# Performance work log

Measured on AMD Instinct MI355X. Metric: run time of the kernel, lower is better.

Reference implementation:

```python
import jax, jax.numpy as jnp
import numpy as np
import math

HIDDEN = 1024
HEADS = 16
HEAD_DIM = HIDDEN // HEADS


def setup_inputs() -> dict:
    key = jax.random.key(0)
    ks = jax.random.split(key, 7)
    B, S = 2, 2048
    scale = 1.0 / math.sqrt(HIDDEN)
    return {
        "x": jax.random.normal(ks[0], (B, S, HIDDEN), dtype=jnp.float32),
        "Wq": jax.random.normal(ks[1], (HIDDEN, HIDDEN), dtype=jnp.float32) * scale,
        "Wk": jax.random.normal(ks[2], (HIDDEN, HIDDEN), dtype=jnp.float32) * scale,
        "Wv": jax.random.normal(ks[3], (HIDDEN, HIDDEN), dtype=jnp.float32) * scale,
        "Wo": jax.random.normal(ks[4], (HIDDEN, HIDDEN), dtype=jnp.float32) * scale,
        "quantum_phase": jax.random.normal(ks[5], (HEADS, HEAD_DIM), dtype=jnp.float32),
        "quantum_amplitude": jnp.ones((HEADS, HEAD_DIM), dtype=jnp.float32),
    }


def reference(x, Wq, Wk, Wv, Wo, quantum_phase, quantum_amplitude):
    B, S, d = x.shape
    H, D = HEADS, HEAD_DIM

    # per-head/per-channel quantum modulation: real(x*exp(i*phase)) == x*cos(phase)
    mod = (jnp.cos(quantum_phase) * quantum_amplitude)[None, :, None, :]  # [1,H,1,D]

    def proj(W):
        return (x @ W).reshape(B, S, H, D).transpose(0, 2, 1, 3)  # [B,H,S,D]

    q = proj(Wq) * mod
    k = proj(Wk) * mod
    v = proj(Wv) * mod

    scores = jnp.einsum("bhid,bhjd->bhij", q, k) / math.sqrt(D)  # [B,H,S,S]

    # quantum interference: scores[i,j] *= cos(2*pi*(i-j)/S)
    idx = jnp.arange(S, dtype=jnp.float32)
    cos_mat = jnp.cos(2.0 * math.pi * (idx[:, None] - idx[None, :]) / S)  # [S,S]
    scores = scores * cos_mat

    w = jax.nn.softmax(scores, axis=-1)
    # superposition of attention weights with key-rolled copy
    w = (w + jnp.roll(w, 1, axis=-1)) / math.sqrt(2.0)

    out = jnp.einsum("bhij,bhjd->bhid", w, v)  # [B,H,S,D]
    out = out.transpose(0, 2, 1, 3).reshape(B, S, d)
    return out @ Wo
```

## Files before the change

kernel.cpp:

```cpp
#include <hip/hip_runtime.h>
#include <hip/hip_bf16.h>
#include <math.h>

#define HIDDEN 1024
#define HEADS  16
#define HDIM   64
#define BATCH  2
#define SEQ    2048
#define ROWS   (BATCH*SEQ)
#define BH     (BATCH*HEADS)

typedef __attribute__((ext_vector_type(8))) short  short8;
typedef __attribute__((ext_vector_type(8))) __bf16 bf16x8;
typedef __attribute__((ext_vector_type(4))) float  f32x4;

static __device__ __forceinline__ unsigned short f2bf(float f) {
    unsigned int u = __builtin_bit_cast(unsigned int, f);
    u += 0x7FFFu + ((u >> 16) & 1u);
    return (unsigned short)(u >> 16);
}
static __device__ __forceinline__ float bf2f(unsigned short h) {
    unsigned int u = ((unsigned int)h) << 16;
    return __builtin_bit_cast(float, u);
}
static __device__ __forceinline__ f32x4 mfma16(short8 a, short8 b, f32x4 c) {
    return __builtin_amdgcn_mfma_f32_16x16x32_bf16(
        __builtin_bit_cast(bf16x8, a), __builtin_bit_cast(bf16x8, b), c, 0, 0, 0);
}
static __device__ __forceinline__ void gl_lds16(const unsigned short* g, unsigned short* l) {
    __builtin_amdgcn_global_load_lds(
        (const __attribute__((address_space(1))) unsigned int*)g,
        (__attribute__((address_space(3))) unsigned int*)l, 16, 0, 0);
}

__global__ __launch_bounds__(256) void prep_kernel(
    const float* __restrict__ x, unsigned short* __restrict__ xb,
    const float* __restrict__ w0, const float* __restrict__ w1,
    const float* __restrict__ w2, const float* __restrict__ w3,
    unsigned short* __restrict__ wt,
    const float* __restrict__ qp, const float* __restrict__ qa,
    float* __restrict__ mod, float* __restrict__ mod2,
    float* __restrict__ posc, float* __restrict__ poss) {
    __shared__ unsigned short tile[64][72];
    const int bid = blockIdx.x;
    const int t = threadIdx.x;
    if (bid < 4096) {
        int i = (bid * 256 + t) * 4;
        float4 v = *(const float4*)(x + i);
        ushort4 o;
        o.x = f2bf(v.x); o.y = f2bf(v.y); o.z = f2bf(v.z); o.w = f2bf(v.w);
        *(ushort4*)(xb + i) = o;
        if (bid < 8) {
            int k = bid * 256 + t;
            if (k < HIDDEN) {
                float m = cosf(qp[k]) * qa[k];
                mod[k] = m;
                mod2[k] = m * m * 0.18033688011112042f;
            }
            if (k < SEQ) {
                float ang = (float)k * (6.283185307179586f / (float)SEQ);
                posc[k] = cosf(ang);
                poss[k] = sinf(ang);
            }
        }
        return;
    }
    int rem = bid - 4096;
    int z = rem >> 8, r2 = rem & 255;
    int n0 = (r2 & 15) * 64, k0 = (r2 >> 4) * 64;
    const float* src = (z == 0) ? w0 : (z == 1) ? w1 : (z == 2) ? w2 : w3;
    unsigned short* dst = wt + (size_t)z * HIDDEN * HIDDEN;
    int cg = t & 15, r0 = t >> 4;
#pragma unroll
    for (int rr = 0; rr < 4; rr++) {
        int kl = r0 + rr * 16;
        float4 v = *(const float4*)(src + (size_t)(k0 + kl) * HIDDEN + n0 + cg * 4);
        tile[cg*4+0][kl] = f2bf(v.x);
        tile[cg*4+1][kl] = f2bf(v.y);
        tile[cg*4+2][kl] = f2bf(v.z);
        tile[cg*4+3][kl] = f2bf(v.w);
    }
    __syncthreads();
#pragma unroll
    for (int rr = 0; rr < 4; rr++) {
        int nl = r0 + rr * 16;
        ushort4 o;
        o.x = tile[nl][cg*4+0]; o.y = tile[nl][cg*4+1];
        o.z = tile[nl][cg*4+2]; o.w = tile[nl][cg*4+3];
        *(ushort4*)(dst + (size_t)(n0 + nl) * HIDDEN + k0 + cg * 4) = o;
    }
}

__global__ __launch_bounds__(256) void gemm_kernel(
    const unsigned short* __restrict__ A, const unsigned short* __restrict__ WtBase,
    unsigned short* __restrict__ CBase, const float* __restrict__ mod) {
    __shared__ unsigned short Alds[128 * 64];
    __shared__ unsigned short Blds[128 * 64];
    const int mode = blockIdx.z;
    const unsigned short* Bt = WtBase + (size_t)mode * HIDDEN * HIDDEN;
    unsigned short* Cout = CBase + (size_t)mode * ROWS * HIDDEN;
    const int m0 = blockIdx.x * 128, n0 = blockIdx.y * 128;
    const int tid = threadIdx.x;
    const int wave = tid >> 6, lane = tid & 63, quad = lane >> 4, l15 = lane & 15;
    const int wr = wave >> 1, wc = wave & 1;
    const int srow = lane >> 3;
    const int schunk = (lane & 7) ^ (srow & 7);

    f32x4 acc[4][4];
    const f32x4 z4 = {0.f, 0.f, 0.f, 0.f};
#pragma unroll
    for (int i = 0; i < 4; i++)
#pragma unroll
        for (int j = 0; j < 4; j++) acc[i][j] = z4;

    for (int k0 = 0; k0 < HIDDEN; k0 += 64) {
#pragma unroll
        for (int p = 0; p < 4; p++) {
            int rbase = p * 32 + wave * 8;
            gl_lds16(A  + (size_t)(m0 + rbase + srow) * HIDDEN + k0 + schunk * 8,
                     &Alds[rbase * 64]);
            gl_lds16(Bt + (size_t)(n0 + rbase + srow) * HIDDEN + k0 + schunk * 8,
                     &Blds[rbase * 64]);
        }
        __syncthreads();
        short8 aF[4][2], bF[4][2];
#pragma unroll
        for (int h = 0; h < 2; h++) {
#pragma unroll
            for (int i = 0; i < 4; i++) {
                int row = wr * 64 + i * 16 + l15;
                aF[i][h] = *(const short8*)(&Alds[row * 64 + ((h * 4 + quad) ^ (l15 & 7)) * 8]);
            }
#pragma unroll
            for (int j = 0; j < 4; j++) {
                int row = wc * 64 + j * 16 + l15;
                bF[j][h] = *(const short8*)(&Blds[row * 64 + ((h * 4 + quad) ^ (l15 & 7)) * 8]);
            }
        }
#pragma unroll
        for (int h = 0; h < 2; h++)
#pragma unroll
            for (int i = 0; i < 4; i++)
#pragma unroll
                for (int j = 0; j < 4; j++)
                    acc[i][j] = mfma16(aF[i][h], bF[j][h], acc[i][j]);
        __syncthreads();
    }

#pragma unroll
    for (int i = 0; i < 4; i++) {
        int mbase = m0 + wr * 64 + i * 16 + quad * 4;
#pragma unroll
        for (int j = 0; j < 4; j++) {
            int n = n0 + wc * 64 + j * 16 + l15;
            float vm = (mode == 2) ? mod[n] : 1.0f;
#pragma unroll
            for (int r = 0; r < 4; r++) {
                int mm = mbase + r;
                Cout[(size_t)mm * HIDDEN + n] = f2bf(acc[i][j][r] * vm);
            }
        }
    }
}

__global__ __launch_bounds__(256) void gemm_o_kernel(
    const unsigned short* __restrict__ A, const unsigned short* __restrict__ Bt,
    float* __restrict__ Out) {
    __shared__ unsigned short Alds[128 * 64];
    __shared__ unsigned short Blds[64 * 64];
    const int m0 = blockIdx.x * 128, n0 = blockIdx.y * 64;
    const int tid = threadIdx.x;
    const int wave = tid >> 6, lane = tid & 63, quad = lane >> 4, l15 = lane & 15;
    const int wr = wave >> 1, wc = wave & 1;
    const int srow = lane >> 3;
    const int schunk = (lane & 7) ^ (srow & 7);

    f32x4 acc[4][2];
    const f32x4 z4 = {0.f, 0.f, 0.f, 0.f};
#pragma unroll
    for (int i = 0; i < 4; i++)
#pragma unroll
        for (int j = 0; j < 2; j++) acc[i][j] = z4;

    for (int k0 = 0; k0 < HIDDEN; k0 += 64) {
#pragma unroll
        for (int p = 0; p < 4; p++) {
            int rbase = p * 32 + wave * 8;
            gl_lds16(A + (size_t)(m0 + rbase + srow) * HIDDEN + k0 + schunk * 8,
                     &Alds[rbase * 64]);
        }
#pragma unroll
        for (int p = 0; p < 2; p++) {
            int rbase = p * 32 + wave * 8;
            gl_lds16(Bt + (size_t)(n0 + rbase + srow) * HIDDEN + k0 + schunk * 8,
                     &Blds[rbase * 64]);
        }
        __syncthreads();
        short8 aF[4][2], bF[2][2];
#pragma unroll
        for (int h = 0; h < 2; h++) {
#pragma unroll
            for (int i = 0; i < 4; i++) {
                int row = wr * 64 + i * 16 + l15;
                aF[i][h] = *(const short8*)(&Alds[row * 64 + ((h * 4 + quad) ^ (l15 & 7)) * 8]);
            }
#pragma unroll
            for (int j = 0; j < 2; j++) {
                int row = wc * 32 + j * 16 + l15;
                bF[j][h] = *(const short8*)(&Blds[row * 64 + ((h * 4 + quad) ^ (l15 & 7)) * 8]);
            }
        }
#pragma unroll
        for (int h = 0; h < 2; h++)
#pragma unroll
            for (int i = 0; i < 4; i++)
#pragma unroll
                for (int j = 0; j < 2; j++)
                    acc[i][j] = mfma16(aF[i][h], bF[j][h], acc[i][j]);
        __syncthreads();
    }

#pragma unroll
    for (int i = 0; i < 4; i++) {
        int mbase = m0 + wr * 64 + i * 16 + quad * 4;
#pragma unroll
        for (int j = 0; j < 2; j++) {
            int n = n0 + wc * 32 + j * 16 + l15;
#pragma unroll
            for (int r = 0; r < 4; r++)
                Out[(size_t)(mbase + r) * HIDDEN + n] = acc[i][j][r];
        }
    }
}

__global__ __launch_bounds__(256) void vshift_kernel(const unsigned short* __restrict__ Vm,
                                                     unsigned short* __restrict__ Vpt) {
    __shared__ unsigned short lds[65][72];
    int bh = blockIdx.x, b = bh >> 4, h = bh & 15;
    int s0 = blockIdx.y * 64;
    int t = threadIdx.x;
    int cg = t & 15, r0 = t >> 4;
#pragma unroll
    for (int rr = 0; rr < 4; rr++) {
        int row = r0 + rr * 16;
        ushort4 v = *(const ushort4*)(Vm + ((size_t)(b * SEQ + s0 + row)) * HIDDEN + h * 64 + cg * 4);
        *(ushort4*)(&lds[row][cg * 4]) = v;
    }
    if (t < 16) {
        int srow = (s0 + 64) & (SEQ - 1);
        ushort4 v = *(const ushort4*)(Vm + ((size_t)(b * SEQ + srow)) * HIDDEN + h * 64 + t * 4);
        *(ushort4*)(&lds[64][t * 4]) = v;
    }
    __syncthreads();
    int d = t & 63, sb = (t >> 6) * 16;
    unsigned short outv[16];
#pragma unroll
    for (int k = 0; k < 16; k++) {
        float a = bf2f(lds[sb + k][d]), bb = bf2f(lds[sb + k + 1][d]);
        outv[k] = f2bf((a + bb) * 0.7071067811865476f);
    }
    unsigned short* dst = Vpt + ((size_t)bh * 64 + d) * SEQ + s0 + sb;
#pragma unroll
    for (int k = 0; k < 16; k += 4) {
        ushort4 o; o.x = outv[k]; o.y = outv[k+1]; o.z = outv[k+2]; o.w = outv[k+3];
        *(ushort4*)(dst + k) = o;
    }
}

#define KT 64
#define PSTR 76
__global__ __launch_bounds__(256) void attn_kernel(const unsigned short* __restrict__ Cq,
                                                   const unsigned short* __restrict__ Ck,
                                                   const unsigned short* __restrict__ Vpt,
                                                   unsigned short* __restrict__ Ob,
                                                   const float* __restrict__ mod2,
                                                   const float* __restrict__ posc,
                                                   const float* __restrict__ poss) {
    __shared__ unsigned short Klds[2][KT * 64];
    __shared__ unsigned short Vtlds[2][64 * 64];
    __shared__ unsigned short Plds[4 * 32 * PSTR];
    const int bh = blockIdx.x;
    const int b = bh >> 4, h = bh & 15;
    const int tid = threadIdx.x, wave = tid >> 6, lane = tid & 63;
    const int quad = lane >> 4, l15 = lane & 15;
    const int q0 = blockIdx.y * 128 + wave * 32;

    short8 qf[2][2];
#pragma unroll
    for (int g = 0; g < 2; g++) {
        int ss = q0 + g * 16 + l15;
        const unsigned short* crow = Cq + ((size_t)(b * SEQ + ss)) * HIDDEN + h * 64;
#pragma unroll
        for (int kk = 0; kk < 2; kk++) {
            int bd = kk * 32 + quad * 8;
            short8 u = *(const short8*)(crow + bd);
            short8 q;
#pragma unroll
            for (int e = 0; e < 8; e++)
                q[e] = (short)f2bf(bf2f((unsigned short)u[e]) * mod2[h * 64 + bd + e]);
            qf[g][kk] = q;
        }
    }
    float ci[2][4], si[2][4];
#pragma unroll
    for (int g = 0; g < 2; g++)
#pragma unroll
        for (int r = 0; r < 4; r++) {
            int ss = q0 + g * 16 + quad * 4 + r;
            ci[g][r] = posc[ss];
            si[g][r] = poss[ss];
        }

    short8 ones;
#pragma unroll
    for (int e = 0; e < 8; e++) ones[e] = (short)0x3F80;

    const f32x4 z4 = {0.f, 0.f, 0.f, 0.f};
    f32x4 acc[2][4], accden[2];
#pragma unroll
    for (int g = 0; g < 2; g++) {
#pragma unroll
        for (int dt = 0; dt < 4; dt++) acc[g][dt] = z4;
        accden[g] = z4;
    }

    unsigned short* pw = &Plds[wave * 32 * PSTR];

    const unsigned short* Kbh = Ck  + ((size_t)b * SEQ) * HIDDEN + h * 64;
    const unsigned short* Vbh = Vpt + (size_t)bh * 64 * SEQ;

    auto stage = [&](int j, int buf) {
#pragma unroll
        for (int p = 0; p < 2; p++) {
            int rb = p * 32 + wave * 8;
            int r  = rb + (lane >> 3);
            int c  = (lane & 7) ^ (r & 7);
            gl_lds16(Kbh + (size_t)(j + r) * HIDDEN + c * 8, &Klds[buf][rb * 64]);
        }
#pragma unroll
        for (int p = 0; p < 2; p++) {
            int rb = p * 32 + wave * 8;
            int r  = rb + (lane >> 3);
            int c  = (lane & 7) ^ (r & 7);
            gl_lds16(Vbh + (size_t)r * SEQ + j + c * 8, &Vtlds[buf][rb * 64]);
        }
    };

    float cjc[4], sjc[4];
#pragma unroll
    for (int t2 = 0; t2 < 4; t2++) {
        int jj = t2 * 16 + l15;
        cjc[t2] = posc[jj]; sjc[t2] = poss[jj];
    }

    stage(0, 0);
    for (int it = 0; it < SEQ / KT; it++) {
        __syncthreads();
        float cjn[4] = {0.f, 0.f, 0.f, 0.f}, sjn[4] = {0.f, 0.f, 0.f, 0.f};
        if (it + 1 < SEQ / KT) {
            stage((it + 1) * KT, (it + 1) & 1);
#pragma unroll
            for (int t2 = 0; t2 < 4; t2++) {
                int jj = (it + 1) * KT + t2 * 16 + l15;
                cjn[t2] = posc[jj]; sjn[t2] = poss[jj];
            }
        }
        const int buf = it & 1;

#pragma unroll
        for (int t2 = 0; t2 < 4; t2++) {
            float cj = cjc[t2], sj = sjc[t2];
            f32x4 sc[2] = {z4, z4};
#pragma unroll
            for (int kk = 0; kk < 2; kk++) {
                int ch = (kk * 4 + quad) ^ (l15 & 7);
                short8 kf = *(const short8*)(&Klds[buf][(t2 * 16 + l15) * 64 + ch * 8]);
#pragma unroll
                for (int g = 0; g < 2; g++)
                    sc[g] = mfma16(qf[g][kk], kf, sc[g]);
            }
#pragma unroll
            for (int g = 0; g < 2; g++) {
#pragma unroll
                for (int r = 0; r < 4; r++) {
                    float w = ci[g][r] * cj + si[g][r] * sj;
                    float p = __builtin_amdgcn_exp2f(sc[g][r] * w);
                    unsigned short pt = (unsigned short)(__builtin_bit_cast(unsigned int, p) >> 16);
                    pw[(g * 16 + quad * 4 + r) * PSTR + t2 * 16 + l15] = pt;
                }
            }
        }

#pragma unroll
        for (int pt = 0; pt < 2; pt++) {
            short8 pa0 = *(const short8*)(&pw[(l15) * PSTR + pt * 32 + quad * 8]);
            short8 pa1 = *(const short8*)(&pw[(16 + l15) * PSTR + pt * 32 + quad * 8]);
            accden[0] = mfma16(pa0, ones, accden[0]);
            accden[1] = mfma16(pa1, ones, accden[1]);
#pragma unroll
            for (int dt = 0; dt < 4; dt++) {
                int ch = (pt * 4 + quad) ^ (l15 & 7);
                short8 vb = *(const short8*)(&Vtlds[buf][(dt * 16 + l15) * 64 + ch * 8]);
                acc[0][dt] = mfma16(pa0, vb, acc[0][dt]);
                acc[1][dt] = mfma16(pa1, vb, acc[1][dt]);
            }
        }
#pragma unroll
        for (int t2 = 0; t2 < 4; t2++) { cjc[t2] = cjn[t2]; sjc[t2] = sjn[t2]; }
    }

#pragma unroll
    for (int g = 0; g < 2; g++) {
        float rinv[4];
#pragma unroll
        for (int r = 0; r < 4; r++) rinv[r] = 1.0f / accden[g][r];
#pragma unroll
        for (int dt = 0; dt < 4; dt++) {
#pragma unroll
            for (int r = 0; r < 4; r++) {
                int q = q0 + g * 16 + quad * 4 + r;
                int d = dt * 16 + l15;
                Ob[((size_t)(b * SEQ + q)) * HIDDEN + h * 64 + d] = f2bf(acc[g][dt][r] * rinv[r]);
            }
        }
    }
}

extern "C" void kernel_launch(void* const* d_in, const int* in_sizes, int n_in,
                              void* d_out, int out_size, void* d_ws, size_t ws_size,
                              hipStream_t stream) {
    const float* x  = (const float*)d_in[0];
    const float* Wq = (const float*)d_in[1];
    const float* Wk = (const float*)d_in[2];
    const float* Wv = (const float*)d_in[3];
    const float* Wo = (const float*)d_in[4];
    const float* qp = (const float*)d_in[5];
    const float* qa = (const float*)d_in[6];
    char* ws = (char*)d_ws;

    unsigned short* Xb  = (unsigned short*)(ws);
    unsigned short* Wt  = (unsigned short*)(ws + (size_t)( 8 << 20));
    unsigned short* Cq  = (unsigned short*)(ws + (size_t)(16 << 20));
    unsigned short* Ck  = (unsigned short*)(ws + (size_t)(24 << 20));
    unsigned short* Cv  = (unsigned short*)(ws + (size_t)(32 << 20));
    unsigned short* Vpt = (unsigned short*)(ws + (size_t)(40 << 20));
    float* mod  = (float*)(ws + (size_t)(48 << 20));
    float* mod2 = mod + 1024;
    float* posc = mod2 + 1024;
    float* poss = posc + 2048;
    float* out  = (float*)d_out;

    prep_kernel<<<5120, 256, 0, stream>>>(x, Xb, Wq, Wk, Wv, Wo, Wt,
                                          qp, qa, mod, mod2, posc, poss);
    gemm_kernel<<<dim3(32, 8, 3), 256, 0, stream>>>(Xb, Wt, Cq, mod);
    vshift_kernel<<<dim3(32, 32), 256, 0, stream>>>(Cv, Vpt);
    attn_kernel<<<dim3(32, 16), 256, 0, stream>>>(Cq, Ck, Vpt, Xb , mod2, posc, poss);
    gemm_o_kernel<<<dim3(32, 16), 256, 0, stream>>>(Xb, Wt + (size_t)3 * HIDDEN * HIDDEN, out);
}
```

Baseline: 246.2 us.

## Double attention key tile to 128 and interleave P writes with PV in 32-key chunks

Raises the key/value tile per iteration from 64 to 128, halving the number of barriers and staging rounds across the sequence. The score/softmax/PV loop is restructured into four 32-key chunks, each writing a small per-wave P buffer and immediately consuming it in PV MFMAs. The V tile swizzle is widened to 16 chunks per row to match. LDS use grows (K and V double buffers doubled) while the P buffer shrinks, which may lower occupancy and adds more register state for the cos/sin vectors.

```diff
diff --git a/kernel.cpp b/kernel.cpp
--- a/kernel.cpp
+++ b/kernel.cpp
@@ -267,8 +267,8 @@
     }
 }
 
-#define KT 64
-#define PSTR 76
+#define KT 128
+#define PSTR2 44
 __global__ __launch_bounds__(256) void attn_kernel(const unsigned short* __restrict__ Cq,
                                                    const unsigned short* __restrict__ Ck,
                                                    const unsigned short* __restrict__ Vpt,
@@ -277,8 +277,8 @@
                                                    const float* __restrict__ posc,
                                                    const float* __restrict__ poss) {
     __shared__ unsigned short Klds[2][KT * 64];
-    __shared__ unsigned short Vtlds[2][64 * 64];
-    __shared__ unsigned short Plds[4 * 32 * PSTR];
+    __shared__ unsigned short Vtlds[2][64 * 128];
+    __shared__ unsigned short Plds[4 * 32 * PSTR2];
     const int bh = blockIdx.x;
     const int b = bh >> 4, h = bh & 15;
     const int tid = threadIdx.x, wave = tid >> 6, lane = tid & 63;
@@ -324,89 +324,93 @@
         accden[g] = z4;
     }
 
-    unsigned short* pw = &Plds[wave * 32 * PSTR];
+    unsigned short* pw = &Plds[wave * 32 * PSTR2];
 
     const unsigned short* Kbh = Ck  + ((size_t)b * SEQ) * HIDDEN + h * 64;
     const unsigned short* Vbh = Vpt + (size_t)bh * 64 * SEQ;
 
     auto stage = [&](int j, int buf) {
 #pragma unroll
-        for (int p = 0; p < 2; p++) {
+        for (int p = 0; p < 4; p++) {
             int rb = p * 32 + wave * 8;
             int r  = rb + (lane >> 3);
             int c  = (lane & 7) ^ (r & 7);
             gl_lds16(Kbh + (size_t)(j + r) * HIDDEN + c * 8, &Klds[buf][rb * 64]);
         }
 #pragma unroll
-        for (int p = 0; p < 2; p++) {
-            int rb = p * 32 + wave * 8;
-            int r  = rb + (lane >> 3);
-            int c  = (lane & 7) ^ (r & 7);
-            gl_lds16(Vbh + (size_t)r * SEQ + j + c * 8, &Vtlds[buf][rb * 64]);
+        for (int p = 0; p < 4; p++) {
+            int rb = p * 16 + wave * 4;
+            int r  = rb + (lane >> 4);
+            int c  = (lane & 15) ^ (r & 15);
+            gl_lds16(Vbh + (size_t)r * SEQ + j + c * 8, &Vtlds[buf][rb * 128]);
         }
     };
 
-    float cjc[4], sjc[4];
-#pragma unroll
-    for (int t2 = 0; t2 < 4; t2++) {
-        int jj = t2 * 16 + l15;
-        cjc[t2] = posc[jj]; sjc[t2] = poss[jj];
+    float cjc[8], sjc[8];
+#pragma unroll
+    for (int tt = 0; tt < 8; tt++) {
+        int jj = tt * 16 + l15;
+        cjc[tt] = posc[jj]; sjc[tt] = poss[jj];
     }
 
     stage(0, 0);
-    for (int it = 0; it < SEQ / KT; it++) {
+    const int NIT = SEQ / KT;
+    for (int it = 0; it < NIT; it++) {
         __syncthreads();
-        float cjn[4] = {0.f, 0.f, 0.f, 0.f}, sjn[4] = {0.f, 0.f, 0.f, 0.f};
-        if (it + 1 < SEQ / KT) {
+        float cjn[8], sjn[8];
+        if (it + 1 < NIT) {
             stage((it + 1) * KT, (it + 1) & 1);
 #pragma unroll
-            for (int t2 = 0; t2 < 4; t2++) {
-                int jj = (it + 1) * KT + t2 * 16 + l15;
-                cjn[t2] = posc[jj]; sjn[t2] = poss[jj];
-            }
+            for (int tt = 0; tt < 8; tt++) {
+                int jj = (it + 1) * KT + tt * 16 + l15;
+                cjn[tt] = posc[jj]; sjn[tt] = poss[jj];
+            }
+        } else {
+#pragma unroll
+            for (int tt = 0; tt < 8; tt++) { cjn[tt] = 0.f; sjn[tt] = 0.f; }
         }
         const int buf = it & 1;
 
 #pragma unroll
-        for (int t2 = 0; t2 < 4; t2++) {
-            float cj = cjc[t2], sj = sjc[t2];
-            f32x4 sc[2] = {z4, z4};
-#pragma unroll
-            for (int kk = 0; kk < 2; kk++) {
-                int ch = (kk * 4 + quad) ^ (l15 & 7);
-                short8 kf = *(const short8*)(&Klds[buf][(t2 * 16 + l15) * 64 + ch * 8]);
-#pragma unroll
-                for (int g = 0; g < 2; g++)
-                    sc[g] = mfma16(qf[g][kk], kf, sc[g]);
-            }
-#pragma unroll
-            for (int g = 0; g < 2; g++) {
-#pragma unroll
-                for (int r = 0; r < 4; r++) {
-                    float w = ci[g][r] * cj + si[g][r] * sj;
-                    float p = __builtin_amdgcn_exp2f(sc[g][r] * w);
-                    unsigned short pt = (unsigned short)(__builtin_bit_cast(unsigned int, p) >> 16);
-                    pw[(g * 16 + quad * 4 + r) * PSTR + t2 * 16 + l15] = pt;
+        for (int chunk = 0; chunk < 4; chunk++) {
+#pragma unroll
+            for (int t2i = 0; t2i < 2; t2i++) {
+                int tt = chunk * 2 + t2i;
+                float cj = cjc[tt], sj = sjc[tt];
+                f32x4 sc[2] = {z4, z4};
+#pragma unroll
+                for (int kk = 0; kk < 2; kk++) {
+                    int ch = (kk * 4 + quad) ^ (l15 & 7);
+                    short8 kf = *(const short8*)(&Klds[buf][(tt * 16 + l15) * 64 + ch * 8]);
+#pragma unroll
+                    for (int g = 0; g < 2; g++)
+                        sc[g] = mfma16(qf[g][kk], kf, sc[g]);
                 }
-            }
-        }
-
-#pragma unroll
-        for (int pt = 0; pt < 2; pt++) {
-            short8 pa0 = *(const short8*)(&pw[(l15) * PSTR + pt * 32 + quad * 8]);
-            short8 pa1 = *(const short8*)(&pw[(16 + l15) * PSTR + pt * 32 + quad * 8]);
+#pragma unroll
+                for (int g = 0; g < 2; g++) {
+#pragma unroll
+                    for (int r = 0; r < 4; r++) {
+                        float w = ci[g][r] * cj + si[g][r] * sj;
+                        float p = __builtin_amdgcn_exp2f(sc[g][r] * w);
+                        unsigned short pt = (unsigned short)(__builtin_bit_cast(unsigned int, p) >> 16);
+                        pw[(g * 16 + quad * 4 + r) * PSTR2 + t2i * 16 + l15] = pt;
+                    }
+                }
+            }
+            short8 pa0 = *(const short8*)(&pw[(l15) * PSTR2 + quad * 8]);
+            short8 pa1 = *(const short8*)(&pw[(16 + l15) * PSTR2 + quad * 8]);
             accden[0] = mfma16(pa0, ones, accden[0]);
             accden[1] = mfma16(pa1, ones, accden[1]);
 #pragma unroll
             for (int dt = 0; dt < 4; dt++) {
-                int ch = (pt * 4 + quad) ^ (l15 & 7);
-                short8 vb = *(const short8*)(&Vtlds[buf][(dt * 16 + l15) * 64 + ch * 8]);
+                int ch = (chunk * 4 + quad) ^ l15;
+                short8 vb = *(const short8*)(&Vtlds[buf][(dt * 16 + l15) * 128 + ch * 8]);
                 acc[0][dt] = mfma16(pa0, vb, acc[0][dt]);
                 acc[1][dt] = mfma16(pa1, vb, acc[1][dt]);
             }
         }
 #pragma unroll
-        for (int t2 = 0; t2 < 4; t2++) { cjc[t2] = cjn[t2]; sjc[t2] = sjn[t2]; }
+        for (int tt = 0; tt < 8; tt++) { cjc[tt] = cjn[tt]; sjc[tt] = sjn[tt]; }
     }
 
 #pragma unroll
```

Measured after the change: 237.7 us. 1.04x faster.
